# Kernel optimization log

Hardware: AMD Instinct MI355X
Metric: run time of the kernel (lower is better)

Reference implementation:

```python
import jax, jax.numpy as jnp
import numpy as np

PERI_IDX = np.array([0, 1, 2, 3, 5, 6, 7, 8])  # non-center taps of the 3x3 window


def _extract_patches(x, stride, padding):
    # x: [B,C,H,W] -> patches [B,C,9,Hout,Wout], tap k = di*3+dj (row-major), matching F.unfold.
    B, C, H, W = x.shape
    Hout = (H + 2 * padding - 3) // stride + 1
    Wout = (W + 2 * padding - 3) // stride + 1
    xp = jnp.pad(x, ((0, 0), (0, 0), (padding, padding), (padding, padding)))
    taps = [xp[:, :, di:di + (Hout - 1) * stride + 1:stride, dj:dj + (Wout - 1) * stride + 1:stride]
            for di in range(3) for dj in range(3)]
    return jnp.stack(taps, axis=2)  # [B,C,9,Hout,Wout]


def setup_inputs() -> dict:
    key = jax.random.key(0)
    k1, k2, k3, k4 = jax.random.split(key, 4)
    B, C, O, H, W = 8, 64, 64, 128, 128
    x = jax.random.normal(k1, (B, C, H, W), dtype=jnp.float32)
    core = jax.random.normal(k2, (O, C, 1, 1), dtype=jnp.float32) * (1.0 / np.sqrt(C))
    periphery = jax.random.uniform(k3, (8,), dtype=jnp.float32, minval=-0.1, maxval=0.1)
    threshold = jnp.array([0.1], dtype=jnp.float32)
    scale = jnp.array([10.0], dtype=jnp.float32)
    return {"x": x, "core": core, "periphery": periphery, "threshold": threshold,
            "scale": scale, "stride": 1, "padding": 1}


def reference(x, core, periphery, threshold, scale, stride, padding):
    B, C, H, W = x.shape
    O = core.shape[0]
    patches = _extract_patches(x, stride, padding)           # [B,C,9,Ho,Wo]
    center = patches[:, :, 4]                                 # [B,C,Ho,Wo]
    # per-pixel variance-like routing statistic over channels and taps
    div = jnp.sum((patches - center[:, :, None]) ** 2, axis=(1, 2))  # [B,Ho,Wo]
    m_hard = jax.nn.sigmoid((div - threshold[0]) * scale[0]) > 0.5   # [B,Ho,Wo] bool
    w = core.reshape(O, C)
    # path 0 (low variance): 1x1 conv on the center pixel
    zero_out = jnp.einsum('bchw,oc->bohw', center, w)
    # path 1 (high variance): periphery-weighted sum then 1x1 conv
    agg = jnp.einsum('bckhw,k->bchw', patches[:, :, PERI_IDX], periphery)
    one_out = jnp.einsum('bchw,oc->bohw', agg, w)
    return jnp.where(m_hard[:, None], one_out, zero_out)
```

## Files before the change

kernel.cpp:

```cpp
#include <hip/hip_runtime.h>
#include <hip/hip_bf16.h>

constexpr int Bc = 8;
constexpr int Cc = 64;
constexpr int Oc = 64;
constexpr int Hc = 128;
constexpr int Wc = 128;
constexpr int HWc = Hc * Wc;
constexpr int CP = 72;

typedef __attribute__((ext_vector_type(8))) short short8;
typedef __attribute__((ext_vector_type(4))) float floatx4;

__global__ __launch_bounds__(512) void spconv_kernel(
    const float* __restrict__ x, const float* __restrict__ core,
    const float* __restrict__ peri, const float* __restrict__ thr,
    const float* __restrict__ scl, float* __restrict__ out)
{
    __shared__ __hip_bfloat16 s_selT[Wc][CP];
    __shared__ __hip_bfloat16 s_core[Oc][CP];
    __shared__ float s_divp[4][Wc];
    __shared__ float s_msk[Wc];
    __shared__ int   s_any;

    const int tid = threadIdx.x;
    const int w   = tid & (Wc - 1);
    const int q   = tid >> 7;
    const int b   = blockIdx.x & 7;
    const int h   = blockIdx.x >> 3;

    if (tid == 0) s_any = 0;

    #pragma unroll
    for (int i = 0; i < 8; ++i) {
        const int idx = i * 512 + tid;
        s_core[idx >> 6][idx & 63] = __float2bfloat16(core[idx]);
    }

    const float* xb = x + (size_t)b * Cc * HWc + (size_t)h * Wc;

    const int   dh[8] = {-1,-1,-1, 0, 0, 1, 1, 1};
    const int   dw[8] = {-1, 0, 1,-1, 1,-1, 0, 1};
    int   off[8];
    float pl[8], mf[8];
    #pragma unroll
    for (int k = 0; k < 8; ++k) {
        const bool okh = (h + dh[k] >= 0) && (h + dh[k] < Hc);
        const bool okw = (w + dw[k] >= 0) && (w + dw[k] < Wc);
        const bool ok  = okh && okw;
        off[k] = ok ? (w + dh[k] * Wc + dw[k]) : w;
        mf[k]  = ok ? 1.f : 0.f;
        pl[k]  = ok ? peri[k] : 0.f;
    }

    float divacc = 0.f;
    const float* rowq = xb + (size_t)(q * 16) * HWc;
    #pragma unroll 4
    for (int ci = 0; ci < 16; ++ci) {
        const float* row = rowq + (size_t)ci * HWc;
        const float t4 = row[w];
        float v[8];
        #pragma unroll
        for (int k = 0; k < 8; ++k) v[k] = row[off[k]];
        float agg = 0.f;
        #pragma unroll
        for (int k = 0; k < 8; ++k) agg = fmaf(pl[k], v[k], agg);
        s_selT[w][q * 16 + ci] = __float2bfloat16(agg);
        #pragma unroll
        for (int k = 0; k < 8; ++k) {
            const float d = fmaf(mf[k], v[k], -t4);
            divacc = fmaf(d, d, divacc);
        }
    }
    s_divp[q][w] = divacc;
    __syncthreads();

    if (tid < Wc) {
        const float div = s_divp[0][tid] + s_divp[1][tid]
                        + s_divp[2][tid] + s_divp[3][tid];
        const bool one = ((div - thr[0]) * scl[0]) > 0.f;
        s_msk[tid] = one ? 1.f : 0.f;
        if (!one) s_any = 1;
    }
    __syncthreads();

    if (s_any) {
        #pragma unroll
        for (int i = 0; i < 16; ++i) {
            const int idx = i * 512 + tid;
            const int ww  = idx & (Wc - 1);
            const int c   = idx >> 7;
            if (s_msk[ww] == 0.f)
                s_selT[ww][c] = __float2bfloat16(xb[(size_t)c * HWc + ww]);
        }
        __syncthreads();
    }

    const int lane = tid & 63;
    const int wid  = tid >> 6;
    const int o0   = (wid & 3) * 16;
    const int wh   = wid >> 2;
    const int n    = lane & 15;
    const int quad = lane >> 4;

    const short8 a0 = *(const short8*)&s_core[o0 + n][quad * 8];
    const short8 a1 = *(const short8*)&s_core[o0 + n][quad * 8 + 32];

    float* outb = out + ((size_t)(b * Oc) * Hc + h) * Wc;

    #pragma unroll
    for (int t = 0; t < 4; ++t) {
        const int w0 = (wh * 4 + t) * 16;
        const short8 b0 = *(const short8*)&s_selT[w0 + n][quad * 8];
        const short8 b1 = *(const short8*)&s_selT[w0 + n][quad * 8 + 32];
        floatx4 acc = {0.f, 0.f, 0.f, 0.f};
        acc = __builtin_amdgcn_mfma_f32_16x16x32_bf16(a0, b0, acc, 0, 0, 0);
        acc = __builtin_amdgcn_mfma_f32_16x16x32_bf16(a1, b1, acc, 0, 0, 0);
        #pragma unroll
        for (int r = 0; r < 4; ++r) {
            const int o = o0 + quad * 4 + r;
            outb[(size_t)o * HWc + w0 + n] = acc[r];
        }
    }
}

extern "C" void kernel_launch(void* const* d_in, const int* in_sizes, int n_in,
                              void* d_out, int out_size, void* d_ws, size_t ws_size,
                              hipStream_t stream) {
    const float* x    = (const float*)d_in[0];
    const float* core = (const float*)d_in[1];
    const float* peri = (const float*)d_in[2];
    const float* thr  = (const float*)d_in[3];
    const float* scl  = (const float*)d_in[4];
    float* out = (float*)d_out;

    spconv_kernel<<<dim3(Bc * Hc), dim3(512), 0, stream>>>(
        x, core, peri, thr, scl, out);
}
```

Before: 102.9 us.

## Process two output rows per block to reuse shared stencil rows

Each block now computes two adjacent output rows, loading four input rows per channel instead of three per output row. The middle rows serve both outputs, which cuts redundant global loads, and the core matrix is staged into shared memory once per two rows. Boundary masks are computed once, the mask/select step is moved after the A-fragment loads, and the launch-bounds occupancy hint is raised. The cost is more shared memory and registers per block and half as many blocks, which may lower parallelism.

```diff
diff --git a/kernel.cpp b/kernel.cpp
--- a/kernel.cpp
+++ b/kernel.cpp
@@ -12,22 +12,23 @@
 typedef __attribute__((ext_vector_type(8))) short short8;
 typedef __attribute__((ext_vector_type(4))) float floatx4;
 
-__global__ __launch_bounds__(512) void spconv_kernel(
+__global__ __launch_bounds__(512, 4) void spconv_kernel(
     const float* __restrict__ x, const float* __restrict__ core,
     const float* __restrict__ peri, const float* __restrict__ thr,
     const float* __restrict__ scl, float* __restrict__ out)
 {
-    __shared__ __hip_bfloat16 s_selT[Wc][CP];
+    __shared__ __hip_bfloat16 s_selT[2][Wc][CP];
     __shared__ __hip_bfloat16 s_core[Oc][CP];
-    __shared__ float s_divp[4][Wc];
-    __shared__ float s_msk[Wc];
+    __shared__ float s_divp[2][4][Wc];
+    __shared__ float s_msk[2][Wc];
     __shared__ int   s_any;
 
     const int tid = threadIdx.x;
     const int w   = tid & (Wc - 1);
     const int q   = tid >> 7;
     const int b   = blockIdx.x & 7;
-    const int h   = blockIdx.x >> 3;
+    const int hp  = blockIdx.x >> 3;
+    const int h0  = hp * 2;
 
     if (tid == 0) s_any = 0;
 
@@ -37,64 +38,83 @@
         s_core[idx >> 6][idx & 63] = __float2bfloat16(core[idx]);
     }
 
-    const float* xb = x + (size_t)b * Cc * HWc + (size_t)h * Wc;
+    const float* xb = x + (size_t)b * Cc * HWc + (size_t)h0 * Wc;
 
-    const int   dh[8] = {-1,-1,-1, 0, 0, 1, 1, 1};
-    const int   dw[8] = {-1, 0, 1,-1, 1,-1, 0, 1};
-    int   off[8];
-    float pl[8], mf[8];
-    #pragma unroll
-    for (int k = 0; k < 8; ++k) {
-        const bool okh = (h + dh[k] >= 0) && (h + dh[k] < Hc);
-        const bool okw = (w + dw[k] >= 0) && (w + dw[k] < Wc);
-        const bool ok  = okh && okw;
-        off[k] = ok ? (w + dh[k] * Wc + dw[k]) : w;
-        mf[k]  = ok ? 1.f : 0.f;
-        pl[k]  = ok ? peri[k] : 0.f;
-    }
+    const float mU  = (h0 > 0) ? 1.f : 0.f;
+    const float mD2 = (h0 < Hc - 2) ? 1.f : 0.f;
+    const int   dU  = (h0 > 0) ? -Wc : 0;
+    const int   dD2 = (h0 < Hc - 2) ? 2 * Wc : Wc;
+    const float mL = (w > 0) ? 1.f : 0.f;
+    const float mR = (w < Wc - 1) ? 1.f : 0.f;
+    const int   oL = (w > 0) ? w - 1 : w;
+    const int   oR = (w < Wc - 1) ? w + 1 : w;
+    const float mUL = mU * mL,  mUR = mU * mR;
+    const float mDL = mD2 * mL, mDR = mD2 * mR;
 
-    float divacc = 0.f;
+    const float p0 = peri[0], p1 = peri[1], p2 = peri[2], p3 = peri[3];
+    const float p4 = peri[4], p5 = peri[5], p6 = peri[6], p7 = peri[7];
+
+    float dvA = 0.f, dvB = 0.f;
     const float* rowq = xb + (size_t)(q * 16) * HWc;
     #pragma unroll 4
     for (int ci = 0; ci < 16; ++ci) {
-        const float* row = rowq + (size_t)ci * HWc;
-        const float t4 = row[w];
-        float v[8];
-        #pragma unroll
-        for (int k = 0; k < 8; ++k) v[k] = row[off[k]];
-        float agg = 0.f;
-        #pragma unroll
-        for (int k = 0; k < 8; ++k) agg = fmaf(pl[k], v[k], agg);
-        s_selT[w][q * 16 + ci] = __float2bfloat16(agg);
-        #pragma unroll
-        for (int k = 0; k < 8; ++k) {
-            const float d = fmaf(mf[k], v[k], -t4);
-            divacc = fmaf(d, d, divacc);
-        }
+        const float* r0 = rowq + (size_t)ci * HWc;
+        const float* rm = r0 + dU;
+        const float* r1 = r0 + Wc;
+        const float* r2 = r0 + dD2;
+
+        float ul = rm[oL], uc = rm[w], ur = rm[oR];
+        float cl = r0[oL], cc = r0[w], cr = r0[oR];
+        float dl = r1[oL], dc = r1[w], dr = r1[oR];
+        float el = r2[oL], ec = r2[w], er = r2[oR];
+
+        ul *= mUL; uc *= mU;  ur *= mUR;
+        const float clm = cl * mL, crm = cr * mR;
+        const float dlm = dl * mL, drm = dr * mR;
+        el *= mDL; ec *= mD2; er *= mDR;
+
+        float aggA =     p0 * ul;
+        aggA = fmaf(p1, uc,  aggA);
+        aggA = fmaf(p2, ur,  aggA);
+        aggA = fmaf(p3, clm, aggA);
+        aggA = fmaf(p4, crm, aggA);
+        aggA = fmaf(p5, dlm, aggA);
+        aggA = fmaf(p6, dc,  aggA);
+        aggA = fmaf(p7, drm, aggA);
+        s_selT[0][w][q * 16 + ci] = __float2bfloat16(aggA);
+
+        float e_;
+        e_ = ul  - cc; dvA = fmaf(e_, e_, dvA);
+        e_ = uc  - cc; dvA = fmaf(e_, e_, dvA);
+        e_ = ur  - cc; dvA = fmaf(e_, e_, dvA);
+        e_ = clm - cc; dvA = fmaf(e_, e_, dvA);
+        e_ = crm - cc; dvA = fmaf(e_, e_, dvA);
+        e_ = dlm - cc; dvA = fmaf(e_, e_, dvA);
+        e_ = dc  - cc; dvA = fmaf(e_, e_, dvA);
+        e_ = drm - cc; dvA = fmaf(e_, e_, dvA);
+
+        float aggB =     p0 * clm;
+        aggB = fmaf(p1, cc,  aggB);
+        aggB = fmaf(p2, crm, aggB);
+        aggB = fmaf(p3, dlm, aggB);
+        aggB = fmaf(p4, drm, aggB);
+        aggB = fmaf(p5, el,  aggB);
+        aggB = fmaf(p6, ec,  aggB);
+        aggB = fmaf(p7, er,  aggB);
+        s_selT[1][w][q * 16 + ci] = __float2bfloat16(aggB);
+
+        e_ = clm - dc; dvB = fmaf(e_, e_, dvB);
+        e_ = cc  - dc; dvB = fmaf(e_, e_, dvB);
+        e_ = crm - dc; dvB = fmaf(e_, e_, dvB);
+        e_ = dlm - dc; dvB = fmaf(e_, e_, dvB);
+        e_ = drm - dc; dvB = fmaf(e_, e_, dvB);
+        e_ = el  - dc; dvB = fmaf(e_, e_, dvB);
+        e_ = ec  - dc; dvB = fmaf(e_, e_, dvB);
+        e_ = er  - dc; dvB = fmaf(e_, e_, dvB);
     }
-    s_divp[q][w] = divacc;
+    s_divp[0][q][w] = dvA;
+    s_divp[1][q][w] = dvB;
     __syncthreads();
-
-    if (tid < Wc) {
-        const float div = s_divp[0][tid] + s_divp[1][tid]
-                        + s_divp[2][tid] + s_divp[3][tid];
-        const bool one = ((div - thr[0]) * scl[0]) > 0.f;
-        s_msk[tid] = one ? 1.f : 0.f;
-        if (!one) s_any = 1;
-    }
-    __syncthreads();
-
-    if (s_any) {
-        #pragma unroll
-        for (int i = 0; i < 16; ++i) {
-            const int idx = i * 512 + tid;
-            const int ww  = idx & (Wc - 1);
-            const int c   = idx >> 7;
-            if (s_msk[ww] == 0.f)
-                s_selT[ww][c] = __float2bfloat16(xb[(size_t)c * HWc + ww]);
-        }
-        __syncthreads();
-    }
 
     const int lane = tid & 63;
     const int wid  = tid >> 6;
@@ -102,24 +122,51 @@
     const int wh   = wid >> 2;
     const int n    = lane & 15;
     const int quad = lane >> 4;
-
     const short8 a0 = *(const short8*)&s_core[o0 + n][quad * 8];
     const short8 a1 = *(const short8*)&s_core[o0 + n][quad * 8 + 32];
 
-    float* outb = out + ((size_t)(b * Oc) * Hc + h) * Wc;
+    if (tid < 2 * Wc) {
+        const int rr = tid >> 7, ww = tid & (Wc - 1);
+        const float div = s_divp[rr][0][ww] + s_divp[rr][1][ww]
+                        + s_divp[rr][2][ww] + s_divp[rr][3][ww];
+        const bool one = ((div - thr[0]) * scl[0]) > 0.f;
+        s_msk[rr][ww] = one ? 1.f : 0.f;
+        if (!one) s_any = 1;
+    }
+    __syncthreads();
+
+    if (s_any) {
+        #pragma unroll
+        for (int i = 0; i < 32; ++i) {
+            const int idx = i * 512 + tid;
+            const int rr  = idx >> 13;
+            const int e2  = idx & 8191;
+            const int ww  = e2 & (Wc - 1);
+            const int c   = e2 >> 7;
+            if (s_msk[rr][ww] == 0.f)
+                s_selT[rr][ww][c] =
+                    __float2bfloat16(xb[(size_t)c * HWc + rr * Wc + ww]);
+        }
+        __syncthreads();
+    }
+
+    float* outb = out + ((size_t)(b * Oc) * Hc + h0) * Wc;
 
     #pragma unroll
-    for (int t = 0; t < 4; ++t) {
-        const int w0 = (wh * 4 + t) * 16;
-        const short8 b0 = *(const short8*)&s_selT[w0 + n][quad * 8];
-        const short8 b1 = *(const short8*)&s_selT[w0 + n][quad * 8 + 32];
-        floatx4 acc = {0.f, 0.f, 0.f, 0.f};
-        acc = __builtin_amdgcn_mfma_f32_16x16x32_bf16(a0, b0, acc, 0, 0, 0);
-        acc = __builtin_amdgcn_mfma_f32_16x16x32_bf16(a1, b1, acc, 0, 0, 0);
+    for (int rr = 0; rr < 2; ++rr) {
         #pragma unroll
-        for (int r = 0; r < 4; ++r) {
-            const int o = o0 + quad * 4 + r;
-            outb[(size_t)o * HWc + w0 + n] = acc[r];
+        for (int t = 0; t < 4; ++t) {
+            const int w0 = (wh * 4 + t) * 16;
+            const short8 b0 = *(const short8*)&s_selT[rr][w0 + n][quad * 8];
+            const short8 b1 = *(const short8*)&s_selT[rr][w0 + n][quad * 8 + 32];
+            floatx4 acc = {0.f, 0.f, 0.f, 0.f};
+            acc = __builtin_amdgcn_mfma_f32_16x16x32_bf16(a0, b0, acc, 0, 0, 0);
+            acc = __builtin_amdgcn_mfma_f32_16x16x32_bf16(a1, b1, acc, 0, 0, 0);
+            #pragma unroll
+            for (int r = 0; r < 4; ++r) {
+                const int o = o0 + quad * 4 + r;
+                outb[(size_t)o * HWc + rr * Wc + w0 + n] = acc[r];
+            }
         }
     }
 }
@@ -134,6 +181,6 @@
     const float* scl  = (const float*)d_in[4];
     float* out = (float*)d_out;
 
-    spconv_kernel<<<dim3(Bc * Hc), dim3(512), 0, stream>>>(
+    spconv_kernel<<<dim3(Bc * Hc / 2), dim3(512), 0, stream>>>(
         x, core, peri, thr, scl, out);
 }
```

New measurement: 100.5 us. 1.02x faster.

## Load stencil rows as float2 and share horizontal neighbors via ds_bpermute

Applied to the files above, without the earlier changes.

The stencil phase is restructured so each lane loads two adjacent pixels per row with vector loads and gets left/right neighbors through cross-lane bpermute, instead of issuing nine scalar loads per channel. Block size drops to 256 threads with each wave doing 16 output channels over all 128 columns. Core weights go directly to bf16 registers, skipping the shared staging copy. The mask check becomes a wave-level vote without the shared flag. This uses a permuted column layout in shared memory, and the swizzled index math plus the extra bpermute traffic add complexity.

```diff
diff --git a/kernel.cpp b/kernel.cpp
--- a/kernel.cpp
+++ b/kernel.cpp
@@ -11,117 +11,165 @@
 
 typedef __attribute__((ext_vector_type(8))) short short8;
 typedef __attribute__((ext_vector_type(4))) float floatx4;
+typedef __attribute__((ext_vector_type(2))) float floatx2;
 
-__global__ __launch_bounds__(512) void spconv_kernel(
+__device__ __forceinline__ float bperm(int idx4, float v) {
+    return __int_as_float(__builtin_amdgcn_ds_bpermute(idx4, __float_as_int(v)));
+}
+__device__ __forceinline__ unsigned cvt_pk_bf16(float lo, float hi) {
+    unsigned r;
+    asm("v_cvt_pk_bf16_f32 %0, %1, %2" : "=v"(r) : "v"(lo), "v"(hi));
+    return r;
+}
+
+__global__ __launch_bounds__(256, 4) void spconv_kernel(
     const float* __restrict__ x, const float* __restrict__ core,
     const float* __restrict__ peri, const float* __restrict__ thr,
     const float* __restrict__ scl, float* __restrict__ out)
 {
     __shared__ __hip_bfloat16 s_selT[Wc][CP];
-    __shared__ __hip_bfloat16 s_core[Oc][CP];
     __shared__ float s_divp[4][Wc];
     __shared__ float s_msk[Wc];
-    __shared__ int   s_any;
 
     const int tid = threadIdx.x;
-    const int w   = tid & (Wc - 1);
-    const int q   = tid >> 7;
+    const int l   = tid & 63;
+    const int wv  = tid >> 6;
     const int b   = blockIdx.x & 7;
     const int h   = blockIdx.x >> 3;
 
-    if (tid == 0) s_any = 0;
+    const int o0   = wv * 16;
+    const int n    = l & 15;
+    const int quad = l >> 4;
 
-    #pragma unroll
-    for (int i = 0; i < 8; ++i) {
-        const int idx = i * 512 + tid;
-        s_core[idx >> 6][idx & 63] = __float2bfloat16(core[idx]);
-    }
+    const float* arow = core + (size_t)(o0 + n) * Cc + quad * 8;
+    const floatx4 af0 = *(const floatx4*)(arow);
+    const floatx4 af1 = *(const floatx4*)(arow + 4);
+    const floatx4 af2 = *(const floatx4*)(arow + 32);
+    const floatx4 af3 = *(const floatx4*)(arow + 36);
+    union { unsigned u[4]; short8 s; } A0, A1;
+    A0.u[0] = cvt_pk_bf16(af0.x, af0.y); A0.u[1] = cvt_pk_bf16(af0.z, af0.w);
+    A0.u[2] = cvt_pk_bf16(af1.x, af1.y); A0.u[3] = cvt_pk_bf16(af1.z, af1.w);
+    A1.u[0] = cvt_pk_bf16(af2.x, af2.y); A1.u[1] = cvt_pk_bf16(af2.z, af2.w);
+    A1.u[2] = cvt_pk_bf16(af3.x, af3.y); A1.u[3] = cvt_pk_bf16(af3.z, af3.w);
 
+    const int upIdx = ((l - 1) & 63) << 2;
+    const int dnIdx = ((l + 1) & 63) << 2;
+    const float lzf = (l == 0)  ? 0.f : 1.f;
+    const float rzf = (l == 63) ? 0.f : 1.f;
+    const float mUf = (h > 0) ? 1.f : 0.f;
+    const float mDf = (h < Hc - 1) ? 1.f : 0.f;
+    const int   dU  = (h > 0) ? -Wc : 0;
+    const int   dD  = (h < Hc - 1) ? Wc : 0;
+
+    const float p0 = peri[0], p1 = peri[1], p2 = peri[2], p3 = peri[3];
+    const float p4 = peri[4], p5 = peri[5], p6 = peri[6], p7 = peri[7];
+    const float thrv = thr[0], sclv = scl[0];
+
+    const float* xw = x + (size_t)b * Cc * HWc + (size_t)h * Wc + 2 * l;
     const float* xb = x + (size_t)b * Cc * HWc + (size_t)h * Wc;
 
-    const int   dh[8] = {-1,-1,-1, 0, 0, 1, 1, 1};
-    const int   dw[8] = {-1, 0, 1,-1, 1,-1, 0, 1};
-    int   off[8];
-    float pl[8], mf[8];
-    #pragma unroll
-    for (int k = 0; k < 8; ++k) {
-        const bool okh = (h + dh[k] >= 0) && (h + dh[k] < Hc);
-        const bool okw = (w + dw[k] >= 0) && (w + dw[k] < Wc);
-        const bool ok  = okh && okw;
-        off[k] = ok ? (w + dh[k] * Wc + dw[k]) : w;
-        mf[k]  = ok ? 1.f : 0.f;
-        pl[k]  = ok ? peri[k] : 0.f;
+    float dlo = 0.f, dhi = 0.f;
+
+#define PROC1(RM, R0, R1, K) do {                                             \
+    const float rmL = lzf * bperm(upIdx, RM.y);                               \
+    const float r0L = lzf * bperm(upIdx, R0.y);                               \
+    const float r1L = lzf * bperm(upIdx, R1.y);                               \
+    const float rmR = rzf * bperm(dnIdx, RM.x);                               \
+    const float r0R = rzf * bperm(dnIdx, R0.x);                               \
+    const float r1R = rzf * bperm(dnIdx, R1.x);                               \
+    { const float t = R0.x;                              \
+      float a = p0 * rmL; a = fmaf(p1, RM.x, a); a = fmaf(p2, RM.y, a);       \
+      a = fmaf(p3, r0L, a); a = fmaf(p4, R0.y, a);                            \
+      a = fmaf(p5, r1L, a); a = fmaf(p6, R1.x, a); a = fmaf(p7, R1.y, a);     \
+      aLo[K] = a; float e;                                                    \
+      e = rmL  - t; dlo = fmaf(e, e, dlo); e = RM.x - t; dlo = fmaf(e, e, dlo); \
+      e = RM.y - t; dlo = fmaf(e, e, dlo); e = r0L  - t; dlo = fmaf(e, e, dlo); \
+      e = R0.y - t; dlo = fmaf(e, e, dlo); e = r1L  - t; dlo = fmaf(e, e, dlo); \
+      e = R1.x - t; dlo = fmaf(e, e, dlo); e = R1.y - t; dlo = fmaf(e, e, dlo); } \
+    { const float t = R0.y;                            \
+      float a = p0 * RM.x; a = fmaf(p1, RM.y, a); a = fmaf(p2, rmR, a);       \
+      a = fmaf(p3, R0.x, a); a = fmaf(p4, r0R, a);                            \
+      a = fmaf(p5, R1.x, a); a = fmaf(p6, R1.y, a); a = fmaf(p7, r1R, a);     \
+      aHi[K] = a; float e;                                                    \
+      e = RM.x - t; dhi = fmaf(e, e, dhi); e = RM.y - t; dhi = fmaf(e, e, dhi); \
+      e = rmR  - t; dhi = fmaf(e, e, dhi); e = R0.x - t; dhi = fmaf(e, e, dhi); \
+      e = r0R  - t; dhi = fmaf(e, e, dhi); e = R1.x - t; dhi = fmaf(e, e, dhi); \
+      e = R1.y - t; dhi = fmaf(e, e, dhi); e = r1R  - t; dhi = fmaf(e, e, dhi); } \
+} while (0)
+
+    #pragma unroll 2
+    for (int j = 0; j < 8; ++j) {
+        const int c0 = wv * 16 + 2 * j;
+        const float* b0p = xw + (size_t)c0 * HWc;
+        const float* b1p = b0p + HWc;
+
+        floatx2 rm0 = *(const floatx2*)(b0p + dU);
+        floatx2 r00 = *(const floatx2*)(b0p);
+        floatx2 r10 = *(const floatx2*)(b0p + dD);
+        floatx2 rm1 = *(const floatx2*)(b1p + dU);
+        floatx2 r01 = *(const floatx2*)(b1p);
+        floatx2 r11 = *(const floatx2*)(b1p + dD);
+        rm0 *= mUf; r10 *= mDf; rm1 *= mUf; r11 *= mDf;
+
+        float aLo[2], aHi[2];
+        PROC1(rm0, r00, r10, 0);
+        PROC1(rm1, r01, r11, 1);
+
+        *(unsigned*)&s_selT[l]      [c0] = cvt_pk_bf16(aLo[0], aLo[1]);
+        *(unsigned*)&s_selT[64 + l] [c0] = cvt_pk_bf16(aHi[0], aHi[1]);
     }
+#undef PROC1
 
-    float divacc = 0.f;
-    const float* rowq = xb + (size_t)(q * 16) * HWc;
-    #pragma unroll 4
-    for (int ci = 0; ci < 16; ++ci) {
-        const float* row = rowq + (size_t)ci * HWc;
-        const float t4 = row[w];
-        float v[8];
-        #pragma unroll
-        for (int k = 0; k < 8; ++k) v[k] = row[off[k]];
-        float agg = 0.f;
-        #pragma unroll
-        for (int k = 0; k < 8; ++k) agg = fmaf(pl[k], v[k], agg);
-        s_selT[w][q * 16 + ci] = __float2bfloat16(agg);
-        #pragma unroll
-        for (int k = 0; k < 8; ++k) {
-            const float d = fmaf(mf[k], v[k], -t4);
-            divacc = fmaf(d, d, divacc);
-        }
-    }
-    s_divp[q][w] = divacc;
-    __syncthreads();
-
-    if (tid < Wc) {
-        const float div = s_divp[0][tid] + s_divp[1][tid]
-                        + s_divp[2][tid] + s_divp[3][tid];
-        const bool one = ((div - thr[0]) * scl[0]) > 0.f;
-        s_msk[tid] = one ? 1.f : 0.f;
-        if (!one) s_any = 1;
+    {
+        floatx2 dv = {dlo, dhi};
+        *(floatx2*)&s_divp[wv][2 * l] = dv;
     }
     __syncthreads();
 
-    if (s_any) {
+    floatx2 sum2 = {0.f, 0.f};
+    #pragma unroll
+    for (int g = 0; g < 4; ++g)
+        sum2 += *(const floatx2*)&s_divp[g][2 * l];
+    const bool badLo = ((sum2.x - thrv) * sclv) <= 0.f;
+    const bool badHi = ((sum2.y - thrv) * sclv) <= 0.f;
+    if (__any(badLo || badHi)) {
+        if (wv == 0) {
+            s_msk[2 * l]     = badLo ? 0.f : 1.f;
+            s_msk[2 * l + 1] = badHi ? 0.f : 1.f;
+        }
+        __syncthreads();
         #pragma unroll
-        for (int i = 0; i < 16; ++i) {
-            const int idx = i * 512 + tid;
-            const int ww  = idx & (Wc - 1);
+        for (int i = 0; i < 32; ++i) {
+            const int idx = i * 256 + tid;
+            const int p   = idx & (Wc - 1);
             const int c   = idx >> 7;
+            const int ww  = ((p & 63) << 1) | (p >> 6);
             if (s_msk[ww] == 0.f)
-                s_selT[ww][c] = __float2bfloat16(xb[(size_t)c * HWc + ww]);
+                s_selT[p][c] = __float2bfloat16(xb[(size_t)c * HWc + ww]);
         }
         __syncthreads();
     }
 
-    const int lane = tid & 63;
-    const int wid  = tid >> 6;
-    const int o0   = (wid & 3) * 16;
-    const int wh   = wid >> 2;
-    const int n    = lane & 15;
-    const int quad = lane >> 4;
-
-    const short8 a0 = *(const short8*)&s_core[o0 + n][quad * 8];
-    const short8 a1 = *(const short8*)&s_core[o0 + n][quad * 8 + 32];
-
     float* outb = out + ((size_t)(b * Oc) * Hc + h) * Wc;
 
+    __builtin_amdgcn_s_setprio(1);
     #pragma unroll
-    for (int t = 0; t < 4; ++t) {
-        const int w0 = (wh * 4 + t) * 16;
-        const short8 b0 = *(const short8*)&s_selT[w0 + n][quad * 8];
-        const short8 b1 = *(const short8*)&s_selT[w0 + n][quad * 8 + 32];
+    for (int t = 0; t < 8; ++t) {
+        const int w0   = t * 16;
+        const int wlog = w0 + n;
+        const int pr   = ((wlog >> 1) & 63) | ((wlog & 1) << 6);
+        const short8 b0 = *(const short8*)&s_selT[pr][quad * 8];
+        const short8 b1 = *(const short8*)&s_selT[pr][quad * 8 + 32];
         floatx4 acc = {0.f, 0.f, 0.f, 0.f};
-        acc = __builtin_amdgcn_mfma_f32_16x16x32_bf16(a0, b0, acc, 0, 0, 0);
-        acc = __builtin_amdgcn_mfma_f32_16x16x32_bf16(a1, b1, acc, 0, 0, 0);
+        acc = __builtin_amdgcn_mfma_f32_16x16x32_bf16(A0.s, b0, acc, 0, 0, 0);
+        acc = __builtin_amdgcn_mfma_f32_16x16x32_bf16(A1.s, b1, acc, 0, 0, 0);
         #pragma unroll
         for (int r = 0; r < 4; ++r) {
             const int o = o0 + quad * 4 + r;
             outb[(size_t)o * HWc + w0 + n] = acc[r];
         }
     }
+    __builtin_amdgcn_s_setprio(0);
 }
 
 extern "C" void kernel_launch(void* const* d_in, const int* in_sizes, int n_in,
@@ -134,6 +182,6 @@
     const float* scl  = (const float*)d_in[4];
     float* out = (float*)d_out;
 
-    spconv_kernel<<<dim3(Bc * Hc), dim3(512), 0, stream>>>(
+    spconv_kernel<<<dim3(Bc * Hc), dim3(256), 0, stream>>>(
         x, core, peri, thr, scl, out);
 }
```

New measurement: 99.78 us. -3.1%, faster.
